# Kernel optimization log

Hardware: AMD Instinct MI355X
Metric: run time of the kernel (lower is better)

The kernel has to match this reference:

```python
import jax, jax.numpy as jnp
import numpy as np

# ---- P4M (D4) group: 8 elements, idx = 4*m + r (m: mirror bit, r: rot90 count) ----
G = 8

def _mr(i):
    return i // 4, i % 4

def _gidx(m, r):
    return 4 * (m % 2) + (r % 4)

def _comp(a, b):
    m1, r1 = _mr(a); m2, r2 = _mr(b)
    return _gidx(m1 + m2, (r1 if m2 == 0 else -r1) + r2)

_INV = [next(b for b in range(G) if _comp(a, b) == 0) for a in range(G)]
# _PERM[h, g] = index of h^{-1} * g  (left regular action on the group axis)
_PERM = np.array([[_comp(_INV[h], g) for g in range(G)] for h in range(G)])


def _spatial_transform(K, h):
    # act on the last two (spatial) kernel axes by group element h = mirror^m rot^r
    m, r = _mr(h)
    if m:
        K = jnp.flip(K, axis=-1)
    return jnp.rot90(K, k=r, axes=(-2, -1))


def _transformed_kernels(W):
    # W: [N_out, N_in, G, k, k] -> [G, N_out, N_in, G, k, k], one kernel per output group element
    return jnp.stack([_spatial_transform(W[:, :, _PERM[h]], h) for h in range(G)])


def conv_gg(x, W, padding):
    # group->group convolution. x: [B, N_in, G, H, W]; W: [N_out, N_in, G, k, k]
    B, Ni, _, H, Wd = x.shape
    No, k = W.shape[0], W.shape[-1]
    K = _transformed_kernels(W).reshape(G * No, Ni * G, k, k)
    y = jax.lax.conv_general_dilated(
        x.reshape(B, Ni * G, H, Wd), K, window_strides=(1, 1),
        padding=[(padding, padding), (padding, padding)],
        dimension_numbers=('NCHW', 'OIHW', 'NCHW'))
    Ho, Wo = y.shape[-2], y.shape[-1]
    return y.reshape(B, G, No, Ho, Wo).transpose(0, 2, 1, 3, 4)  # [B, N_out, G, Ho, Wo]


def channel_att_gg(x, W1, W2):
    # squeeze-excite over (channel, group) with group-equivariant weight sharing
    s = x.mean(axis=(-2, -1))                                  # [B, C, G]
    P1 = W1[:, :, _PERM]                                       # [M, C, G_out, G_in]
    t = jax.nn.relu(jnp.einsum('mcog,bcg->bmo', P1, s))        # [B, M, G]
    P2 = W2[:, :, _PERM]                                       # [C, M, G_out, G_in]
    return jax.nn.sigmoid(jnp.einsum('cmog,bmg->bco', P2, t))  # [B, C, G]


def spatial_att_gg(x, Wsp):
    # CBAM-style: mean/max over channels, group-equivariant 7x7 conv, sigmoid
    p = jnp.stack([x.mean(axis=1), x.max(axis=1)], axis=1)     # [B, 2, G, H, W]
    return jax.nn.sigmoid(conv_gg(p, Wsp, padding=Wsp.shape[-1] // 2))  # [B, 1, G, H, W]


def f_att_conv_gg(x, W, Wc1, Wc2, Wsp, padding):
    a_ch = channel_att_gg(x, Wc1, Wc2)[:, :, :, None, None]
    a_sp = spatial_att_gg(x, Wsp)
    return conv_gg(x * a_ch * a_sp, W, padding)


def bn3d(x, gamma, beta, eps=2e-5):
    # training-mode BatchNorm3d: stats over (B, G, H, W) per channel, biased variance
    mu = x.mean(axis=(0, 2, 3, 4), keepdims=True)
    var = ((x - mu) ** 2).mean(axis=(0, 2, 3, 4), keepdims=True)
    return (x - mu) * jax.lax.rsqrt(var + eps) * gamma[None, :, None, None, None] \
        + beta[None, :, None, None, None]


C, MID, K, SPK, B, H = 96, 48, 3, 7, 4, 56  # MID = C // ratio-reduction (ratio = C//2)


def setup_inputs() -> dict:
    key = jax.random.key(0)
    ks = jax.random.split(key, 12)
    def rn(k, shape, scale):
        return jax.random.normal(k, shape, dtype=jnp.float32) * scale
    wsc = float(np.sqrt(2.0 / (C * G * K * K)))
    asc = float(np.sqrt(2.0 / (C * G)))
    ssc = float(np.sqrt(2.0 / (2 * G * SPK * SPK)))
    return {
        'x': rn(ks[0], (B, C, G, H, H), 1.0),
        'bn1_gamma': jnp.ones((C,), jnp.float32), 'bn1_beta': jnp.zeros((C,), jnp.float32),
        'bn2_gamma': jnp.ones((C,), jnp.float32), 'bn2_beta': jnp.zeros((C,), jnp.float32),
        'c1_W': rn(ks[1], (C, C, G, K, K), wsc),
        'c1_att1': rn(ks[2], (MID, C, G), asc), 'c1_att2': rn(ks[3], (C, MID, G), asc),
        'c1_sp': rn(ks[4], (1, 2, G, SPK, SPK), ssc),
        'c2_W': rn(ks[5], (C, C, G, K, K), wsc),
        'c2_att1': rn(ks[6], (MID, C, G), asc), 'c2_att2': rn(ks[7], (C, MID, G), asc),
        'c2_sp': rn(ks[8], (1, 2, G, SPK, SPK), ssc),
    }


def reference(x, bn1_gamma, bn1_beta, bn2_gamma, bn2_beta,
              c1_W, c1_att1, c1_att2, c1_sp,
              c2_W, c2_att1, c2_att2, c2_sp):
    # fiber_map='id', stride=1 -> no group pooling, identity shortcut
    h = f_att_conv_gg(jax.nn.relu(bn3d(x, bn1_gamma, bn1_beta)),
                      c1_W, c1_att1, c1_att2, c1_sp, padding=1)
    h = f_att_conv_gg(jax.nn.relu(bn3d(h, bn2_gamma, bn2_beta)),
                      c2_W, c2_att1, c2_att2, c2_sp, padding=1)
    return x + h
```

## Files before the change

kernel.cpp:

```cpp
#include <hip/hip_runtime.h>
#include <math.h>

#define NG 8
#define C96 96
#define NMID 48
#define HW 56
#define PIX 3136
#define GHW 25088
#define CIN 768
#define NPIXT 9633792
#define BN_N 100352
#define PADW 58
#define PADPIX 3364
#define WTK 589824
#define PPL 3968

typedef __attribute__((ext_vector_type(8))) short bf16x8;
typedef __attribute__((ext_vector_type(4))) float f32x4;

__device__ __forceinline__ int d_comp(int a, int b){
  int m1=a>>2, r1=a&3, m2=b>>2, r2=b&3;
  int m=(m1+m2)&1;
  int r = (m2==0) ? (r1+r2) : (r2-r1);
  r = (r+4)&3;
  return 4*m+r;
}
__device__ __forceinline__ int d_inv(int a){ return (a>>2) ? a : ((4-(a&3))&3); }
__device__ __forceinline__ int d_perm(int h, int g){ return d_comp(d_inv(h), g); }

__device__ __forceinline__ void d_src(int h, int dy, int dx, int n, int* sy, int* sx){
  int r=h&3, m=h>>2, e=n-1;
  int y,x;
  if(r==0){y=dy; x=dx;}
  else if(r==1){y=dx; x=e-dy;}
  else if(r==2){y=e-dy; x=e-dx;}
  else {y=e-dx; x=dy;}
  if(m) x = e-x;
  *sy=y; *sx=x;
}

__device__ __forceinline__ unsigned short f2bf(float f){
  unsigned int u = __builtin_bit_cast(unsigned int, f);
  unsigned int r = (u + 0x7FFFu + ((u>>16)&1u)) >> 16;
  return (unsigned short)r;
}

__device__ __forceinline__ void gload_lds16(const void* g, void* l){
  __builtin_amdgcn_global_load_lds((const __attribute__((address_space(1))) unsigned int*)g,
                                   (__attribute__((address_space(3))) unsigned int*)l, 16, 0, 0);
}

#define VMCNT0() asm volatile("s_waitcnt vmcnt(0)" ::: "memory")
#define BAR() do { __builtin_amdgcn_s_barrier(); __builtin_amdgcn_sched_barrier(0); } while(0)

__global__ void k_bn_stats(const float* __restrict__ in, float* __restrict__ spart){
  __shared__ float sm[8];
  int c = blockIdx.x, s = blockIdx.y;
  int b = s>>1, half = s&1;
  const float4* p = (const float4*)(in + ((size_t)(b*C96 + c))*GHW) + half*(GHW/8);
  float sum=0.f, sum2=0.f;
  for (int i=threadIdx.x; i<GHW/8; i+=256){
    float4 v = p[i];
    sum  += v.x+v.y+v.z+v.w;
    sum2 += v.x*v.x+v.y*v.y+v.z*v.z+v.w*v.w;
  }
  #pragma unroll
  for (int off=32; off>0; off>>=1){ sum += __shfl_down(sum,off); sum2 += __shfl_down(sum2,off); }
  int lane=threadIdx.x&63, wid=threadIdx.x>>6;
  if(lane==0){ sm[wid]=sum; sm[4+wid]=sum2; }
  __syncthreads();
  if(threadIdx.x==0){
    float a=sm[0]+sm[1]+sm[2]+sm[3], b2=sm[4]+sm[5]+sm[6]+sm[7];
    spart[(c*8+s)*2]   = a;
    spart[(c*8+s)*2+1] = b2;
  }
}

__global__ __launch_bounds__(256) void k_fuse1(const float* __restrict__ in,
    const float* __restrict__ spart, const float* __restrict__ gamma, const float* __restrict__ beta,
    float* __restrict__ work, float* __restrict__ pp){
  __shared__ float scs[C96], shs[C96];
  int tid = threadIdx.x;
  if (tid < C96){
    float s=0.f, s2=0.f;
    #pragma unroll
    for (int k=0;k<8;k++){ s += spart[(tid*8+k)*2]; s2 += spart[(tid*8+k)*2+1]; }
    float mean = s*(1.f/BN_N);
    float var  = s2*(1.f/BN_N) - mean*mean;
    float sc = gamma[tid]*rsqrtf(var + 2e-5f);
    scs[tid] = sc; shs[tid] = beta[tid] - mean*sc;
  }
  __syncthreads();
  int bg = blockIdx.y; int b = bg>>3, g = bg&7;
  int px = blockIdx.x*256 + tid;
  if (px >= PIX) return;
  float pm = 0.f, pmx = 0.f;
  for (int c = 0; c < C96; c++){
    size_t idx = ((size_t)((b*C96 + c)*8 + g))*PIX + px;
    float v = fmaxf(fmaf(in[idx], scs[c], shs[c]), 0.f);
    work[idx] = v;
    pm += v; pmx = fmaxf(pmx, v);
  }
  int y = px/HW, x = px - y*HW;
  pp[(size_t)(b*16 + g)*PPL     + (y+3)*64 + (x+3)] = pm;
  pp[(size_t)(b*16 + 8 + g)*PPL + (y+3)*64 + (x+3)] = pmx;
}

__global__ void k_chan_stats(const float* __restrict__ t, float* __restrict__ s){
  int bcg = blockIdx.x;
  const float4* p = (const float4*)(t + (size_t)bcg*PIX);
  float acc=0.f;
  for (int i=threadIdx.x; i<PIX/4; i+=64){ float4 v=p[i]; acc += v.x+v.y+v.z+v.w; }
  #pragma unroll
  for(int off=32;off>0;off>>=1) acc += __shfl_down(acc,off);
  if(threadIdx.x==0) s[bcg] = acc * (1.f/3136.f);
}

__global__ void k_ca(const float* __restrict__ sbuf, const float* __restrict__ W1,
                     const float* __restrict__ W2, float* __restrict__ ach){
  __shared__ float sl[CIN], tl[NMID*8];
  int b = blockIdx.x, tid = threadIdx.x;
  sl[tid] = sbuf[b*CIN + tid];
  __syncthreads();
  int o = tid & 7;
  int pg[8];
  #pragma unroll
  for (int g=0; g<8; g++) pg[g] = d_perm(o, g);
  if (tid < NMID*8){
    int m = tid >> 3;
    float acc = 0.f;
    for (int c=0; c<C96; c++){
      #pragma unroll
      for (int g=0; g<8; g++) acc += W1[(m*C96+c)*8+pg[g]] * sl[c*8+g];
    }
    tl[tid] = fmaxf(acc, 0.f);
  }
  __syncthreads();
  {
    int c = tid >> 3;
    float acc = 0.f;
    for (int m=0; m<NMID; m++){
      #pragma unroll
      for (int g=0; g<8; g++) acc += W2[(c*NMID+m)*8+pg[g]] * tl[(m<<3)+g];
    }
    ach[b*CIN + tid] = 1.f/(1.f+__expf(-acc));
  }
}

__global__ __launch_bounds__(256) void k_sp_conv(const float* __restrict__ pp,
    const float* __restrict__ Wsp, float* __restrict__ aspt){
  __shared__ float wl[2*8*49];
  int bh = blockIdx.y; int b=bh>>3, h=bh&7;
  for(int idx=threadIdx.x; idx<784; idx+=256){
    int i = idx/392; int rem = idx-i*392;
    int g = rem/49; int kk = rem-g*49;
    int dy=kk/7, dx=kk-dy*7;
    int pg = d_perm(h,g);
    int sy,sx; d_src(h,dy,dx,7,&sy,&sx);
    wl[idx] = Wsp[(i*8+pg)*49 + sy*7+sx] * (i==0 ? (1.f/96.f) : 1.f);
  }
  __syncthreads();
  int pix = blockIdx.x*256 + threadIdx.x;
  if(pix>=PIX) return;
  int y=pix/HW, x=pix-y*HW;
  const float* base = pp + (size_t)(b*16)*PPL + y*64 + x;
  float acc=0.f;
  for(int ig=0; ig<16; ig++){
    const float* pb = base + (size_t)ig*PPL;
    const float* wb = wl + ig*49;
    #pragma unroll
    for(int dy=0; dy<7; dy++){
      #pragma unroll
      for(int dx=0; dx<7; dx++)
        acc = fmaf(pb[dy*64+dx], wb[dy*7+dx], acc);
    }
  }
  aspt[((size_t)b*PIX + pix)*8 + h] = 1.f/(1.f+__expf(-acc));
}

__global__ void k_zero(uint4* __restrict__ xp, uint4* __restrict__ pp){
  size_t i = (size_t)blockIdx.x*256 + threadIdx.x;
  uint4 z = (uint4){0u,0u,0u,0u};
  if (i < 1291392) xp[i] = z;
  else { size_t j = i - 1291392; if (j < 63488) pp[j] = z; }
}

__global__ __launch_bounds__(256) void k_mod_t(const float* __restrict__ work,
    const float* __restrict__ ach, const float* __restrict__ aspt,
    unsigned int* __restrict__ XpU){
  __shared__ float tile[64][65];
  int b = blockIdx.z;
  int cg0 = blockIdx.y*64;
  int pix0 = blockIdx.x*64;
  int lane = threadIdx.x & 63, w = threadIdx.x >> 6;
  for (int r = w; r < 64; r += 4){
    int cg = cg0 + r;
    float a1 = ach[b*CIN + cg];
    tile[r][lane] = work[(size_t)(b*CIN + cg)*PIX + pix0 + lane] * a1;
  }
  __syncthreads();
  int half = lane >> 5;
  int cgA = (lane & 31)*2;
  #pragma unroll
  for (int it = 0; it < 8; it++){
    int p = it*8 + w*2 + half;
    int pix = pix0 + p;
    int y = pix/HW, x = pix - y*HW;
    float2 a2 = *(const float2*)(aspt + ((size_t)b*PIX + pix)*8 + (cgA&7));
    float vA = tile[cgA][p]   * a2.x;
    float vB = tile[cgA+1][p] * a2.y;
    unsigned int u = (unsigned int)f2bf(vA) | ((unsigned int)f2bf(vB) << 16);
    XpU[(((size_t)b*PADPIX + (y+1)*PADW + (x+1))*CIN + cg0 + cgA) >> 1] = u;
  }
}

__global__ void k_ktb2(const float* __restrict__ W1src, const float* __restrict__ W2src,
                       unsigned short* __restrict__ Wt1, unsigned short* __restrict__ Wt2){
  const float* W = blockIdx.y ? W2src : W1src;
  unsigned short* Wt = blockIdx.y ? Wt2 : Wt1;
  int idx = blockIdx.x*256 + threadIdx.x;
  int ci = idx % CIN;
  int t2 = idx / CIN;
  int co = t2 % CIN;
  int kk = t2 / CIN;
  int h = co/C96, o = co - h*C96;
  int i = ci >> 3, g = ci & 7;
  int dy = kk/3, dx = kk - dy*3;
  int sy, sx; d_src(h, dy, dx, 3, &sy, &sx);
  float v = W[((o*C96 + i)*8 + d_perm(h,g))*9 + sy*3 + sx];
  Wt[idx] = f2bf(v);
}

__global__ __launch_bounds__(256, 2) void k_convmf(const unsigned short* __restrict__ Xp,
    const unsigned short* __restrict__ Wt, const float* __restrict__ resid,
    float* __restrict__ out){
  __shared__ unsigned short lds[40960];
  int tid = threadIdx.x, lane = tid & 63, w = tid >> 6;
  int col = lane & 15, kg = lane >> 4;

  int bid = blockIdx.x;
  int wgid = (bid & 7)*56 + (bid >> 3);
  int m = wgid/112; int rem = wgid - m*112;
  int b = rem/28;  int rp = rem - b*28;
  int y0 = rp*2, co0 = m*192;

  int xgo[8], xds[8];
  #pragma unroll
  for (int t = 0; t < 8; t++){
    int fg = (w*8 + t)*64 + lane;
    int row = fg >> 9;
    int pr  = (fg >> 3) & 63;
    int gi  = fg & 7;
    int sg  = gi ^ (pr & 7);
    xgo[t] = (b*PADPIX + (y0+row)*PADW + pr)*CIN + sg*8;
    xds[t] = (w*8 + t)*512;
  }
  int wgo[6], wofs[6];
  {
    int crow = lane >> 3, gi = lane & 7, sg = gi ^ crow;
    #pragma unroll
    for (int j = 0; j < 6; j++){
      int cb = w*48 + j*8;
      wgo[j]  = (co0 + cb + crow)*CIN + sg*8;
      wofs[j] = cb*64;
    }
  }
  int aidx[3][2];
  #pragma unroll
  for (int mf = 0; mf < 3; mf++)
    #pragma unroll
    for (int ks = 0; ks < 2; ks++)
      aidx[mf][ks] = (w*48 + mf*16 + col)*64 + ((((ks<<2)|kg) ^ (col&7)) << 3);

  int qx[7], qyl[7];
  #pragma unroll
  for (int nf = 0; nf < 7; nf++){
    int q = nf*16 + col;
    qyl[nf] = (q >= 56) ? 1 : 0;
    qx[nf]  = q - 56*qyl[nf];
  }

  f32x4 acc[3][7];
  #pragma unroll
  for (int mf=0; mf<3; mf++)
    #pragma unroll
    for (int nf=0; nf<7; nf++)
      acc[mf][nf] = (f32x4){0.f,0.f,0.f,0.f};

  #pragma unroll
  for (int j = 0; j < 6; j++) gload_lds16(Wt + wgo[j], &lds[16384 + wofs[j]]);
  #pragma unroll
  for (int t = 0; t < 8; t++) gload_lds16(Xp + xgo[t], &lds[xds[t]]);
  VMCNT0();
  BAR();

  int q = 0;
  for (int chunk = 0; chunk < 12; chunk++){
    int ci0 = chunk << 6;
    for (int kk = 0; kk < 9; kk++){
      int s = chunk*9 + kk;
      const unsigned short* Wb = &lds[16384 + q*12288];
      bf16x8 A[3][2];
      #pragma unroll
      for (int mf=0; mf<3; mf++)
        #pragma unroll
        for (int ks=0; ks<2; ks++)
          A[mf][ks] = *(const bf16x8*)(Wb + aidx[mf][ks]);
      if (s <= 106){
        int kk2 = kk + 1, c2 = chunk;
        if (kk2 == 9){ kk2 = 0; c2++; }
        size_t gofs = (size_t)kk2*WTK + (c2 << 6);
        int dofs = 16384 + (q^1)*12288;
        #pragma unroll
        for (int j = 0; j < 6; j++) gload_lds16(Wt + gofs + wgo[j], &lds[dofs + wofs[j]]);
      }
      int dyk = kk/3, dxk = kk - dyk*3;
      __builtin_amdgcn_s_setprio(1);
      #pragma unroll
      for (int nf = 0; nf < 7; nf++){
        int t1 = qx[nf] + dxk;
        int i0 = ((qyl[nf]+dyk) << 12) | (t1 << 6) | ((kg ^ (t1 & 7)) << 3);
        bf16x8 B0 = *(const bf16x8*)(lds + i0);
        bf16x8 B1 = *(const bf16x8*)(lds + (i0 ^ 32));
        acc[0][nf] = __builtin_amdgcn_mfma_f32_16x16x32_bf16(A[0][0], B0, acc[0][nf], 0,0,0);
        acc[1][nf] = __builtin_amdgcn_mfma_f32_16x16x32_bf16(A[1][0], B0, acc[1][nf], 0,0,0);
        acc[2][nf] = __builtin_amdgcn_mfma_f32_16x16x32_bf16(A[2][0], B0, acc[2][nf], 0,0,0);
        acc[0][nf] = __builtin_amdgcn_mfma_f32_16x16x32_bf16(A[0][1], B1, acc[0][nf], 0,0,0);
        acc[1][nf] = __builtin_amdgcn_mfma_f32_16x16x32_bf16(A[1][1], B1, acc[1][nf], 0,0,0);
        acc[2][nf] = __builtin_amdgcn_mfma_f32_16x16x32_bf16(A[2][1], B1, acc[2][nf], 0,0,0);
      }
      __builtin_amdgcn_s_setprio(0);
      VMCNT0();
      BAR();
      if (kk == 8 && chunk < 11){
        #pragma unroll
        for (int t = 0; t < 8; t++) gload_lds16(Xp + xgo[t] + ci0 + 64, &lds[xds[t]]);
        VMCNT0();
        BAR();
      }
      q ^= 1;
    }
  }

  #pragma unroll
  for (int mf = 0; mf < 3; mf++){
    int co_b = co0 + w*48 + mf*16;
    int h = co_b/C96;
    int ob = co_b - h*C96 + kg*4;
    #pragma unroll
    for (int nf = 0; nf < 7; nf++){
      int qq = nf*16 + col;
      #pragma unroll
      for (int r = 0; r < 4; r++){
        size_t oi = ((size_t)((b*C96 + ob + r)*8 + h))*PIX + y0*56 + qq;
        float v = acc[mf][nf][r];
        if (resid) v += resid[oi];
        out[oi] = v;
      }
    }
  }
}

static void run_layer(const float* bn_in, float* work,
                      const float* a1W, const float* a2W, const float* spW,
                      const float* bng, const float* bnb,
                      const float* resid, float* convout,
                      float* spart, float* sbuf, float* ach, float* ppP, float* aspt,
                      unsigned short* Wt, unsigned short* Xp, hipStream_t stream)
{
  k_bn_stats<<<dim3(C96,8),256,0,stream>>>(bn_in, spart);
  k_fuse1<<<dim3(13,32),256,0,stream>>>(bn_in, spart, bng, bnb, work, ppP);
  k_chan_stats<<<4*C96*NG,64,0,stream>>>(work, sbuf);
  k_ca<<<4,CIN,0,stream>>>(sbuf, a1W, a2W, ach);
  k_sp_conv<<<dim3(13,32),256,0,stream>>>(ppP, spW, aspt);
  k_mod_t<<<dim3(PIX/64, CIN/64, 4),256,0,stream>>>(work, ach, aspt, (unsigned int*)Xp);
  k_convmf<<<448,256,0,stream>>>(Xp, Wt, resid, convout);
}

extern "C" void kernel_launch(void* const* d_in, const int* in_sizes, int n_in,
                              void* d_out, int out_size, void* d_ws, size_t ws_size,
                              hipStream_t stream) {
  const float* x    = (const float*)d_in[0];
  const float* bn1g = (const float*)d_in[1];
  const float* bn1b = (const float*)d_in[2];
  const float* bn2g = (const float*)d_in[3];
  const float* bn2b = (const float*)d_in[4];
  const float* c1W  = (const float*)d_in[5];
  const float* c1a1 = (const float*)d_in[6];
  const float* c1a2 = (const float*)d_in[7];
  const float* c1sp = (const float*)d_in[8];
  const float* c2W  = (const float*)d_in[9];
  const float* c2a1 = (const float*)d_in[10];
  const float* c2a2 = (const float*)d_in[11];
  const float* c2sp = (const float*)d_in[12];
  float* out = (float*)d_out;
  float* ws  = (float*)d_ws;

  float* bufA = ws;
  unsigned short* Wt1 = (unsigned short*)(bufA + NPIXT);
  unsigned short* Wt2 = Wt1 + 9*CIN*CIN;
  unsigned short* Xp  = Wt2 + 9*CIN*CIN;
  float* spart = (float*)(Xp + (size_t)4*PADPIX*CIN);
  float* sbuf  = spart + 1536;
  float* ach   = sbuf + 4*C96*NG;
  float* ppP   = ach + 4*C96*NG;
  float* aspt  = ppP + 4*16*PPL;

  k_ktb2<<<dim3((9*CIN*CIN)/256, 2),256,0,stream>>>(c1W, c2W, Wt1, Wt2);
  k_zero<<<5293,256,0,stream>>>((uint4*)Xp, (uint4*)ppP);

  run_layer(x, bufA, c1a1, c1a2, c1sp, bn1g, bn1b, nullptr, bufA,
            spart, sbuf, ach, ppP, aspt, Wt1, Xp, stream);
  run_layer(bufA, bufA, c2a1, c2a2, c2sp, bn2g, bn2b, x, out,
            spart, sbuf, ach, ppP, aspt, Wt2, Xp, stream);
}
```

Before: 556.0 us.

## Stream conv weights from global into registers and fuse channel-mean into BN kernel

The conv kernel no longer stages weights through LDS. Each wave loads its A fragments straight from global memory into registers one tap ahead, and the input tile is double-buffered in LDS with a prefetch at tap 6. This cuts the per-tap barrier down to one per chunk. Separately, the per-(b,c,g) channel mean is now accumulated with wave reductions and atomics inside k_fuse1, which removes the k_chan_stats pass that re-read the full activation tensor. The risks are exposed global-load latency on weights, extra register pressure, and atomic contention.

```diff
diff --git a/kernel.cpp b/kernel.cpp
--- a/kernel.cpp
+++ b/kernel.cpp
@@ -53,10 +53,12 @@
 #define VMCNT0() asm volatile("s_waitcnt vmcnt(0)" ::: "memory")
 #define BAR() do { __builtin_amdgcn_s_barrier(); __builtin_amdgcn_sched_barrier(0); } while(0)
 
-__global__ void k_bn_stats(const float* __restrict__ in, float* __restrict__ spart){
+__global__ void k_bn_stats(const float* __restrict__ in, float* __restrict__ spart,
+                           float* __restrict__ sbuf){
   __shared__ float sm[8];
   int c = blockIdx.x, s = blockIdx.y;
   int b = s>>1, half = s&1;
+  if (threadIdx.x < 4) sbuf[((b*C96 + c)<<3) + ((s&1)<<2) + threadIdx.x] = 0.f;
   const float4* p = (const float4*)(in + ((size_t)(b*C96 + c))*GHW) + half*(GHW/8);
   float sum=0.f, sum2=0.f;
   for (int i=threadIdx.x; i<GHW/8; i+=256){
@@ -78,7 +80,7 @@
 
 __global__ __launch_bounds__(256) void k_fuse1(const float* __restrict__ in,
     const float* __restrict__ spart, const float* __restrict__ gamma, const float* __restrict__ beta,
-    float* __restrict__ work, float* __restrict__ pp){
+    float* __restrict__ work, float* __restrict__ pp, float* __restrict__ sbuf){
   __shared__ float scs[C96], shs[C96];
   int tid = threadIdx.x;
   if (tid < C96){
@@ -94,33 +96,28 @@
   int bg = blockIdx.y; int b = bg>>3, g = bg&7;
   int px = blockIdx.x*256 + tid;
   if (px >= PIX) return;
+  int lane = tid & 63;
   float pm = 0.f, pmx = 0.f;
   for (int c = 0; c < C96; c++){
     size_t idx = ((size_t)((b*C96 + c)*8 + g))*PIX + px;
     float v = fmaxf(fmaf(in[idx], scs[c], shs[c]), 0.f);
     work[idx] = v;
     pm += v; pmx = fmaxf(pmx, v);
+    float r = v;
+    #pragma unroll
+    for (int off=32; off>0; off>>=1) r += __shfl_down(r, off);
+    if (lane == 0) atomicAdd(&sbuf[(b*C96 + c)*8 + g], r);
   }
   int y = px/HW, x = px - y*HW;
   pp[(size_t)(b*16 + g)*PPL     + (y+3)*64 + (x+3)] = pm;
   pp[(size_t)(b*16 + 8 + g)*PPL + (y+3)*64 + (x+3)] = pmx;
-}
-
-__global__ void k_chan_stats(const float* __restrict__ t, float* __restrict__ s){
-  int bcg = blockIdx.x;
-  const float4* p = (const float4*)(t + (size_t)bcg*PIX);
-  float acc=0.f;
-  for (int i=threadIdx.x; i<PIX/4; i+=64){ float4 v=p[i]; acc += v.x+v.y+v.z+v.w; }
-  #pragma unroll
-  for(int off=32;off>0;off>>=1) acc += __shfl_down(acc,off);
-  if(threadIdx.x==0) s[bcg] = acc * (1.f/3136.f);
 }
 
 __global__ void k_ca(const float* __restrict__ sbuf, const float* __restrict__ W1,
                      const float* __restrict__ W2, float* __restrict__ ach){
   __shared__ float sl[CIN], tl[NMID*8];
   int b = blockIdx.x, tid = threadIdx.x;
-  sl[tid] = sbuf[b*CIN + tid];
+  sl[tid] = sbuf[b*CIN + tid] * (1.f/3136.f);
   __syncthreads();
   int o = tid & 7;
   int pg[8];
@@ -234,7 +231,7 @@
 __global__ __launch_bounds__(256, 2) void k_convmf(const unsigned short* __restrict__ Xp,
     const unsigned short* __restrict__ Wt, const float* __restrict__ resid,
     float* __restrict__ out){
-  __shared__ unsigned short lds[40960];
+  __shared__ unsigned short lds[32768];
   int tid = threadIdx.x, lane = tid & 63, w = tid >> 6;
   int col = lane & 15, kg = lane >> 4;
 
@@ -255,29 +252,23 @@
     xgo[t] = (b*PADPIX + (y0+row)*PADW + pr)*CIN + sg*8;
     xds[t] = (w*8 + t)*512;
   }
-  int wgo[6], wofs[6];
-  {
-    int crow = lane >> 3, gi = lane & 7, sg = gi ^ crow;
-    #pragma unroll
-    for (int j = 0; j < 6; j++){
-      int cb = w*48 + j*8;
-      wgo[j]  = (co0 + cb + crow)*CIN + sg*8;
-      wofs[j] = cb*64;
-    }
-  }
-  int aidx[3][2];
-  #pragma unroll
-  for (int mf = 0; mf < 3; mf++)
-    #pragma unroll
-    for (int ks = 0; ks < 2; ks++)
-      aidx[mf][ks] = (w*48 + mf*16 + col)*64 + ((((ks<<2)|kg) ^ (col&7)) << 3);
-
-  int qx[7], qyl[7];
-  #pragma unroll
-  for (int nf = 0; nf < 7; nf++){
+
+  const unsigned short* abase[3];
+  #pragma unroll
+  for (int mf=0; mf<3; mf++)
+    abase[mf] = Wt + (size_t)(co0 + w*48 + mf*16 + col)*CIN + kg*8;
+
+  int boff[3][7];
+  #pragma unroll
+  for (int nf=0; nf<7; nf++){
     int q = nf*16 + col;
-    qyl[nf] = (q >= 56) ? 1 : 0;
-    qx[nf]  = q - 56*qyl[nf];
+    int qyl = (q >= 56) ? 1 : 0;
+    int qx = q - 56*qyl;
+    #pragma unroll
+    for (int dx=0; dx<3; dx++){
+      int t1 = qx + dx;
+      boff[dx][nf] = (qyl<<12) | (t1<<6) | ((kg ^ (t1&7))<<3);
+    }
   }
 
   f32x4 acc[3][7];
@@ -288,57 +279,65 @@
       acc[mf][nf] = (f32x4){0.f,0.f,0.f,0.f};
 
   #pragma unroll
-  for (int j = 0; j < 6; j++) gload_lds16(Wt + wgo[j], &lds[16384 + wofs[j]]);
-  #pragma unroll
   for (int t = 0; t < 8; t++) gload_lds16(Xp + xgo[t], &lds[xds[t]]);
+  bf16x8 Ac[3][2];
+  #pragma unroll
+  for (int mf=0; mf<3; mf++)
+    #pragma unroll
+    for (int ks=0; ks<2; ks++)
+      Ac[mf][ks] = *(const bf16x8*)(abase[mf] + ks*32);
   VMCNT0();
   BAR();
 
-  int q = 0;
   for (int chunk = 0; chunk < 12; chunk++){
     int ci0 = chunk << 6;
+    const unsigned short* Xc = lds + (chunk&1)*16384;
+    #pragma unroll
     for (int kk = 0; kk < 9; kk++){
-      int s = chunk*9 + kk;
-      const unsigned short* Wb = &lds[16384 + q*12288];
-      bf16x8 A[3][2];
+      bf16x8 An[3][2];
+      if (kk < 8){
+        #pragma unroll
+        for (int mf=0; mf<3; mf++)
+          #pragma unroll
+          for (int ks=0; ks<2; ks++)
+            An[mf][ks] = *(const bf16x8*)(abase[mf] + (kk+1)*WTK + ci0 + ks*32);
+      }
+      if (kk == 6 && chunk < 11){
+        #pragma unroll
+        for (int t = 0; t < 8; t++)
+          gload_lds16(Xp + xgo[t] + ci0 + 64, &lds[(((chunk&1)^1)<<14) + xds[t]]);
+      }
+      int dyk = kk/3, dxk = kk - dyk*3;
+      __builtin_amdgcn_s_setprio(1);
+      #pragma unroll
+      for (int nf = 0; nf < 7; nf++){
+        int idx = boff[dxk][nf] + (dyk<<12);
+        bf16x8 B0 = *(const bf16x8*)(Xc + idx);
+        bf16x8 B1 = *(const bf16x8*)(Xc + (idx^32));
+        acc[0][nf] = __builtin_amdgcn_mfma_f32_16x16x32_bf16(Ac[0][0], B0, acc[0][nf], 0,0,0);
+        acc[1][nf] = __builtin_amdgcn_mfma_f32_16x16x32_bf16(Ac[1][0], B0, acc[1][nf], 0,0,0);
+        acc[2][nf] = __builtin_amdgcn_mfma_f32_16x16x32_bf16(Ac[2][0], B0, acc[2][nf], 0,0,0);
+        acc[0][nf] = __builtin_amdgcn_mfma_f32_16x16x32_bf16(Ac[0][1], B1, acc[0][nf], 0,0,0);
+        acc[1][nf] = __builtin_amdgcn_mfma_f32_16x16x32_bf16(Ac[1][1], B1, acc[1][nf], 0,0,0);
+        acc[2][nf] = __builtin_amdgcn_mfma_f32_16x16x32_bf16(Ac[2][1], B1, acc[2][nf], 0,0,0);
+      }
+      __builtin_amdgcn_s_setprio(0);
+      if (kk < 8){
+        #pragma unroll
+        for (int mf=0; mf<3; mf++)
+          #pragma unroll
+          for (int ks=0; ks<2; ks++)
+            Ac[mf][ks] = An[mf][ks];
+      }
+    }
+    if (chunk < 11){
+      VMCNT0();
+      BAR();
       #pragma unroll
       for (int mf=0; mf<3; mf++)
         #pragma unroll
         for (int ks=0; ks<2; ks++)
-          A[mf][ks] = *(const bf16x8*)(Wb + aidx[mf][ks]);
-      if (s <= 106){
-        int kk2 = kk + 1, c2 = chunk;
-        if (kk2 == 9){ kk2 = 0; c2++; }
-        size_t gofs = (size_t)kk2*WTK + (c2 << 6);
-        int dofs = 16384 + (q^1)*12288;
-        #pragma unroll
-        for (int j = 0; j < 6; j++) gload_lds16(Wt + gofs + wgo[j], &lds[dofs + wofs[j]]);
-      }
-      int dyk = kk/3, dxk = kk - dyk*3;
-      __builtin_amdgcn_s_setprio(1);
-      #pragma unroll
-      for (int nf = 0; nf < 7; nf++){
-        int t1 = qx[nf] + dxk;
-        int i0 = ((qyl[nf]+dyk) << 12) | (t1 << 6) | ((kg ^ (t1 & 7)) << 3);
-        bf16x8 B0 = *(const bf16x8*)(lds + i0);
-        bf16x8 B1 = *(const bf16x8*)(lds + (i0 ^ 32));
-        acc[0][nf] = __builtin_amdgcn_mfma_f32_16x16x32_bf16(A[0][0], B0, acc[0][nf], 0,0,0);
-        acc[1][nf] = __builtin_amdgcn_mfma_f32_16x16x32_bf16(A[1][0], B0, acc[1][nf], 0,0,0);
-        acc[2][nf] = __builtin_amdgcn_mfma_f32_16x16x32_bf16(A[2][0], B0, acc[2][nf], 0,0,0);
-        acc[0][nf] = __builtin_amdgcn_mfma_f32_16x16x32_bf16(A[0][1], B1, acc[0][nf], 0,0,0);
-        acc[1][nf] = __builtin_amdgcn_mfma_f32_16x16x32_bf16(A[1][1], B1, acc[1][nf], 0,0,0);
-        acc[2][nf] = __builtin_amdgcn_mfma_f32_16x16x32_bf16(A[2][1], B1, acc[2][nf], 0,0,0);
-      }
-      __builtin_amdgcn_s_setprio(0);
-      VMCNT0();
-      BAR();
-      if (kk == 8 && chunk < 11){
-        #pragma unroll
-        for (int t = 0; t < 8; t++) gload_lds16(Xp + xgo[t] + ci0 + 64, &lds[xds[t]]);
-        VMCNT0();
-        BAR();
-      }
-      q ^= 1;
+          Ac[mf][ks] = *(const bf16x8*)(abase[mf] + ci0 + 64 + ks*32);
     }
   }
 
@@ -368,9 +367,8 @@
                       float* spart, float* sbuf, float* ach, float* ppP, float* aspt,
                       unsigned short* Wt, unsigned short* Xp, hipStream_t stream)
 {
-  k_bn_stats<<<dim3(C96,8),256,0,stream>>>(bn_in, spart);
-  k_fuse1<<<dim3(13,32),256,0,stream>>>(bn_in, spart, bng, bnb, work, ppP);
-  k_chan_stats<<<4*C96*NG,64,0,stream>>>(work, sbuf);
+  k_bn_stats<<<dim3(C96,8),256,0,stream>>>(bn_in, spart, sbuf);
+  k_fuse1<<<dim3(13,32),256,0,stream>>>(bn_in, spart, bng, bnb, work, ppP, sbuf);
   k_ca<<<4,CIN,0,stream>>>(sbuf, a1W, a2W, ach);
   k_sp_conv<<<dim3(13,32),256,0,stream>>>(ppP, spW, aspt);
   k_mod_t<<<dim3(PIX/64, CIN/64, 4),256,0,stream>>>(work, ach, aspt, (unsigned int*)Xp);
```

After: 912.8 us. 1.64x slower.

## Recompute BN+ReLU on the fly instead of materializing activations; unroll conv loop

Applied to the files above, without the earlier changes.

The normalized and ReLU'd activation tensor is no longer written to memory. The pooling, channel-stat and modulation kernels each recompute the BN affine and ReLU from the raw input and the partial statistics, which removes a full-tensor write and the reads of it. Separately, the MFMA conv main loop is restructured into a fully unrolled 18-step body over pairs of chunks, with precomputed LDS offsets so per-iteration index arithmetic goes away. The cost is redundant BN recompute in three kernels and more register pressure from the precomputed offset tables.

```diff
diff --git a/kernel.cpp b/kernel.cpp
--- a/kernel.cpp
+++ b/kernel.cpp
@@ -14,6 +14,7 @@
 #define PADPIX 3364
 #define WTK 589824
 #define PPL 3968
+#define WBASE 16384
 
 typedef __attribute__((ext_vector_type(8))) short bf16x8;
 typedef __attribute__((ext_vector_type(4))) float f32x4;
@@ -76,9 +77,9 @@
   }
 }
 
-__global__ __launch_bounds__(256) void k_fuse1(const float* __restrict__ in,
+__global__ __launch_bounds__(256) void k_pool(const float* __restrict__ in,
     const float* __restrict__ spart, const float* __restrict__ gamma, const float* __restrict__ beta,
-    float* __restrict__ work, float* __restrict__ pp){
+    float* __restrict__ pp){
   __shared__ float scs[C96], shs[C96];
   int tid = threadIdx.x;
   if (tid < C96){
@@ -98,7 +99,6 @@
   for (int c = 0; c < C96; c++){
     size_t idx = ((size_t)((b*C96 + c)*8 + g))*PIX + px;
     float v = fmaxf(fmaf(in[idx], scs[c], shs[c]), 0.f);
-    work[idx] = v;
     pm += v; pmx = fmaxf(pmx, v);
   }
   int y = px/HW, x = px - y*HW;
@@ -106,14 +106,27 @@
   pp[(size_t)(b*16 + 8 + g)*PPL + (y+3)*64 + (x+3)] = pmx;
 }
 
-__global__ void k_chan_stats(const float* __restrict__ t, float* __restrict__ s){
+__global__ void k_chan(const float* __restrict__ in, const float* __restrict__ spart,
+    const float* __restrict__ gamma, const float* __restrict__ beta, float* __restrict__ sout){
   int bcg = blockIdx.x;
-  const float4* p = (const float4*)(t + (size_t)bcg*PIX);
+  int c = (bcg >> 3) % C96;
+  float s=0.f, s2=0.f;
+  #pragma unroll
+  for (int k=0;k<8;k++){ s += spart[(c*8+k)*2]; s2 += spart[(c*8+k)*2+1]; }
+  float mean = s*(1.f/BN_N);
+  float var  = s2*(1.f/BN_N) - mean*mean;
+  float sc = gamma[c]*rsqrtf(var + 2e-5f);
+  float sh = beta[c] - mean*sc;
+  const float4* p = (const float4*)(in + (size_t)bcg*PIX);
   float acc=0.f;
-  for (int i=threadIdx.x; i<PIX/4; i+=64){ float4 v=p[i]; acc += v.x+v.y+v.z+v.w; }
+  for (int i=threadIdx.x; i<PIX/4; i+=64){
+    float4 v = p[i];
+    acc += fmaxf(fmaf(v.x,sc,sh),0.f) + fmaxf(fmaf(v.y,sc,sh),0.f)
+         + fmaxf(fmaf(v.z,sc,sh),0.f) + fmaxf(fmaf(v.w,sc,sh),0.f);
+  }
   #pragma unroll
   for(int off=32;off>0;off>>=1) acc += __shfl_down(acc,off);
-  if(threadIdx.x==0) s[bcg] = acc * (1.f/3136.f);
+  if(threadIdx.x==0) sout[bcg] = acc * (1.f/3136.f);
 }
 
 __global__ void k_ca(const float* __restrict__ sbuf, const float* __restrict__ W1,
@@ -185,18 +198,34 @@
   else { size_t j = i - 1291392; if (j < 63488) pp[j] = z; }
 }
 
-__global__ __launch_bounds__(256) void k_mod_t(const float* __restrict__ work,
+__global__ __launch_bounds__(256) void k_mod_t(const float* __restrict__ in,
+    const float* __restrict__ spart, const float* __restrict__ gamma, const float* __restrict__ beta,
     const float* __restrict__ ach, const float* __restrict__ aspt,
     unsigned int* __restrict__ XpU){
   __shared__ float tile[64][65];
+  __shared__ float scs8[8], shs8[8];
   int b = blockIdx.z;
   int cg0 = blockIdx.y*64;
   int pix0 = blockIdx.x*64;
-  int lane = threadIdx.x & 63, w = threadIdx.x >> 6;
+  int tid = threadIdx.x;
+  if (tid < 8){
+    int c = (cg0>>3) + tid;
+    float s=0.f, s2=0.f;
+    #pragma unroll
+    for (int k=0;k<8;k++){ s += spart[(c*8+k)*2]; s2 += spart[(c*8+k)*2+1]; }
+    float mean = s*(1.f/BN_N);
+    float var  = s2*(1.f/BN_N) - mean*mean;
+    float sc = gamma[c]*rsqrtf(var + 2e-5f);
+    scs8[tid] = sc; shs8[tid] = beta[c] - mean*sc;
+  }
+  __syncthreads();
+  int lane = tid & 63, w = tid >> 6;
   for (int r = w; r < 64; r += 4){
     int cg = cg0 + r;
     float a1 = ach[b*CIN + cg];
-    tile[r][lane] = work[(size_t)(b*CIN + cg)*PIX + pix0 + lane] * a1;
+    float raw = in[(size_t)(b*CIN + cg)*PIX + pix0 + lane];
+    float v = fmaxf(fmaf(raw, scs8[r>>3], shs8[r>>3]), 0.f);
+    tile[r][lane] = v * a1;
   }
   __syncthreads();
   int half = lane >> 5;
@@ -265,19 +294,27 @@
       wofs[j] = cb*64;
     }
   }
-  int aidx[3][2];
-  #pragma unroll
-  for (int mf = 0; mf < 3; mf++)
-    #pragma unroll
-    for (int ks = 0; ks < 2; ks++)
-      aidx[mf][ks] = (w*48 + mf*16 + col)*64 + ((((ks<<2)|kg) ^ (col&7)) << 3);
-
-  int qx[7], qyl[7];
-  #pragma unroll
-  for (int nf = 0; nf < 7; nf++){
-    int q = nf*16 + col;
-    qyl[nf] = (q >= 56) ? 1 : 0;
-    qx[nf]  = q - 56*qyl[nf];
+  int ab[2][3][2];
+  #pragma unroll
+  for (int q = 0; q < 2; q++)
+    #pragma unroll
+    for (int mf = 0; mf < 3; mf++)
+      #pragma unroll
+      for (int ks = 0; ks < 2; ks++)
+        ab[q][mf][ks] = WBASE + q*12288 + (w*48 + mf*16 + col)*64 + ((((ks<<2)|kg) ^ (col&7)) << 3);
+
+  int boff[3][7], boff2[3][7];
+  #pragma unroll
+  for (int nf=0; nf<7; nf++){
+    int q2 = nf*16 + col;
+    int qyl = (q2 >= 56) ? 1 : 0;
+    int qx = q2 - 56*qyl;
+    #pragma unroll
+    for (int dx=0; dx<3; dx++){
+      int t1 = qx + dx;
+      boff[dx][nf]  = (qyl<<12) | (t1<<6) | ((kg ^ (t1&7))<<3);
+      boff2[dx][nf] = boff[dx][nf] ^ 32;
+    }
   }
 
   f32x4 acc[3][7];
@@ -288,57 +325,58 @@
       acc[mf][nf] = (f32x4){0.f,0.f,0.f,0.f};
 
   #pragma unroll
-  for (int j = 0; j < 6; j++) gload_lds16(Wt + wgo[j], &lds[16384 + wofs[j]]);
+  for (int j = 0; j < 6; j++) gload_lds16(Wt + wgo[j], &lds[WBASE + wofs[j]]);
   #pragma unroll
   for (int t = 0; t < 8; t++) gload_lds16(Xp + xgo[t], &lds[xds[t]]);
   VMCNT0();
   BAR();
 
-  int q = 0;
-  for (int chunk = 0; chunk < 12; chunk++){
-    int ci0 = chunk << 6;
-    for (int kk = 0; kk < 9; kk++){
-      int s = chunk*9 + kk;
-      const unsigned short* Wb = &lds[16384 + q*12288];
-      bf16x8 A[3][2];
-      #pragma unroll
-      for (int mf=0; mf<3; mf++)
+  for (int cc = 0; cc < 6; cc++){
+    #pragma unroll
+    for (int t = 0; t < 18; t++){
+      const int ch = t/9;
+      const int kk = t - ch*9;
+      const int q  = t & 1;
+      const int dyk = kk/3, dxk = kk - dyk*3;
+      bf16x8 A00 = *(const bf16x8*)(lds + ab[q][0][0]);
+      bf16x8 A01 = *(const bf16x8*)(lds + ab[q][0][1]);
+      bf16x8 A10 = *(const bf16x8*)(lds + ab[q][1][0]);
+      bf16x8 A11 = *(const bf16x8*)(lds + ab[q][1][1]);
+      bf16x8 A20 = *(const bf16x8*)(lds + ab[q][2][0]);
+      bf16x8 A21 = *(const bf16x8*)(lds + ab[q][2][1]);
+      if (t < 17 || cc < 5){
+        const int tn = t + 1;
+        const int chn = tn/9;
+        const int kk2 = tn - chn*9;
+        const unsigned short* wsrc = Wt + (size_t)kk2*WTK + cc*128 + chn*64;
         #pragma unroll
-        for (int ks=0; ks<2; ks++)
-          A[mf][ks] = *(const bf16x8*)(Wb + aidx[mf][ks]);
-      if (s <= 106){
-        int kk2 = kk + 1, c2 = chunk;
-        if (kk2 == 9){ kk2 = 0; c2++; }
-        size_t gofs = (size_t)kk2*WTK + (c2 << 6);
-        int dofs = 16384 + (q^1)*12288;
-        #pragma unroll
-        for (int j = 0; j < 6; j++) gload_lds16(Wt + gofs + wgo[j], &lds[dofs + wofs[j]]);
+        for (int j = 0; j < 6; j++)
+          gload_lds16(wsrc + wgo[j], &lds[WBASE + (q^1)*12288 + wofs[j]]);
       }
-      int dyk = kk/3, dxk = kk - dyk*3;
+      const int dyo = dyk << 12;
       __builtin_amdgcn_s_setprio(1);
       #pragma unroll
       for (int nf = 0; nf < 7; nf++){
-        int t1 = qx[nf] + dxk;
-        int i0 = ((qyl[nf]+dyk) << 12) | (t1 << 6) | ((kg ^ (t1 & 7)) << 3);
-        bf16x8 B0 = *(const bf16x8*)(lds + i0);
-        bf16x8 B1 = *(const bf16x8*)(lds + (i0 ^ 32));
-        acc[0][nf] = __builtin_amdgcn_mfma_f32_16x16x32_bf16(A[0][0], B0, acc[0][nf], 0,0,0);
-        acc[1][nf] = __builtin_amdgcn_mfma_f32_16x16x32_bf16(A[1][0], B0, acc[1][nf], 0,0,0);
-        acc[2][nf] = __builtin_amdgcn_mfma_f32_16x16x32_bf16(A[2][0], B0, acc[2][nf], 0,0,0);
-        acc[0][nf] = __builtin_amdgcn_mfma_f32_16x16x32_bf16(A[0][1], B1, acc[0][nf], 0,0,0);
-        acc[1][nf] = __builtin_amdgcn_mfma_f32_16x16x32_bf16(A[1][1], B1, acc[1][nf], 0,0,0);
-        acc[2][nf] = __builtin_amdgcn_mfma_f32_16x16x32_bf16(A[2][1], B1, acc[2][nf], 0,0,0);
+        bf16x8 B0 = *(const bf16x8*)(lds + boff[dxk][nf]  + dyo);
+        bf16x8 B1 = *(const bf16x8*)(lds + boff2[dxk][nf] + dyo);
+        acc[0][nf] = __builtin_amdgcn_mfma_f32_16x16x32_bf16(A00, B0, acc[0][nf], 0,0,0);
+        acc[1][nf] = __builtin_amdgcn_mfma_f32_16x16x32_bf16(A10, B0, acc[1][nf], 0,0,0);
+        acc[2][nf] = __builtin_amdgcn_mfma_f32_16x16x32_bf16(A20, B0, acc[2][nf], 0,0,0);
+        acc[0][nf] = __builtin_amdgcn_mfma_f32_16x16x32_bf16(A01, B1, acc[0][nf], 0,0,0);
+        acc[1][nf] = __builtin_amdgcn_mfma_f32_16x16x32_bf16(A11, B1, acc[1][nf], 0,0,0);
+        acc[2][nf] = __builtin_amdgcn_mfma_f32_16x16x32_bf16(A21, B1, acc[2][nf], 0,0,0);
       }
       __builtin_amdgcn_s_setprio(0);
       VMCNT0();
       BAR();
-      if (kk == 8 && chunk < 11){
+      if (t == 8 || (t == 17 && cc < 5)){
+        const int next = (t == 8) ? 1 : 2;
+        const unsigned short* xsrc = Xp + cc*128 + next*64;
         #pragma unroll
-        for (int t = 0; t < 8; t++) gload_lds16(Xp + xgo[t] + ci0 + 64, &lds[xds[t]]);
+        for (int tt = 0; tt < 8; tt++) gload_lds16(xsrc + xgo[tt], &lds[xds[tt]]);
         VMCNT0();
         BAR();
       }
-      q ^= 1;
     }
   }
 
@@ -361,7 +399,7 @@
   }
 }
 
-static void run_layer(const float* bn_in, float* work,
+static void run_layer(const float* bn_in,
                       const float* a1W, const float* a2W, const float* spW,
                       const float* bng, const float* bnb,
                       const float* resid, float* convout,
@@ -369,11 +407,11 @@
                       unsigned short* Wt, unsigned short* Xp, hipStream_t stream)
 {
   k_bn_stats<<<dim3(C96,8),256,0,stream>>>(bn_in, spart);
-  k_fuse1<<<dim3(13,32),256,0,stream>>>(bn_in, spart, bng, bnb, work, ppP);
-  k_chan_stats<<<4*C96*NG,64,0,stream>>>(work, sbuf);
+  k_pool<<<dim3(13,32),256,0,stream>>>(bn_in, spart, bng, bnb, ppP);
+  k_chan<<<4*C96*NG,64,0,stream>>>(bn_in, spart, bng, bnb, sbuf);
   k_ca<<<4,CIN,0,stream>>>(sbuf, a1W, a2W, ach);
   k_sp_conv<<<dim3(13,32),256,0,stream>>>(ppP, spW, aspt);
-  k_mod_t<<<dim3(PIX/64, CIN/64, 4),256,0,stream>>>(work, ach, aspt, (unsigned int*)Xp);
+  k_mod_t<<<dim3(PIX/64, CIN/64, 4),256,0,stream>>>(bn_in, spart, bng, bnb, ach, aspt, (unsigned int*)Xp);
   k_convmf<<<448,256,0,stream>>>(Xp, Wt, resid, convout);
 }
 
@@ -409,8 +447,8 @@
   k_ktb2<<<dim3((9*CIN*CIN)/256, 2),256,0,stream>>>(c1W, c2W, Wt1, Wt2);
   k_zero<<<5293,256,0,stream>>>((uint4*)Xp, (uint4*)ppP);
 
-  run_layer(x, bufA, c1a1, c1a2, c1sp, bn1g, bn1b, nullptr, bufA,
+  run_layer(x, c1a1, c1a2, c1sp, bn1g, bn1b, nullptr, bufA,
             spart, sbuf, ach, ppP, aspt, Wt1, Xp, stream);
-  run_layer(bufA, bufA, c2a1, c2a2, c2sp, bn2g, bn2b, x, out,
+  run_layer(bufA, c2a1, c2a2, c2sp, bn2g, bn2b, x, out,
             spart, sbuf, ach, ppP, aspt, Wt2, Xp, stream);
 }
```

Result: no change. 555.9 us (-0.0%).
